# Kernel tuning notes

Measured on AMD Instinct MI355X. Metric: run time of the kernel, lower is better.

The kernel has to match this reference:

```python
import jax, jax.numpy as jnp
import numpy as np

D_MODEL = 1024
H = 16
D_K = D_MODEL // H


def setup_inputs() -> dict:
    key = jax.random.key(0)
    ks = jax.random.split(key, 12)
    B, S = 2, 2048
    inp = {
        "q": jax.random.normal(ks[0], (B, S, D_MODEL), jnp.float32),
        "k": jax.random.normal(ks[1], (B, S, D_MODEL), jnp.float32),
        "v": jax.random.normal(ks[2], (B, S, D_MODEL), jnp.float32),
        "mask": jax.random.randint(ks[3], (1, 1, S, S), 0, 2, jnp.int32),
    }
    s = 1.0 / np.sqrt(D_MODEL)
    inp["wq_w"] = jax.random.normal(ks[4], (D_MODEL, D_MODEL), jnp.float32) * s
    inp["wq_b"] = jnp.zeros((D_MODEL,), jnp.float32)
    inp["wk_w"] = jax.random.normal(ks[5], (D_MODEL, D_MODEL), jnp.float32) * s
    inp["wk_b"] = jnp.zeros((D_MODEL,), jnp.float32)
    inp["wv_w"] = jax.random.normal(ks[6], (D_MODEL, D_MODEL), jnp.float32) * s
    inp["wv_b"] = jnp.zeros((D_MODEL,), jnp.float32)
    inp["wo_w"] = jax.random.normal(ks[7], (D_MODEL, D_MODEL), jnp.float32) * s
    inp["wo_b"] = jnp.zeros((D_MODEL,), jnp.float32)
    return inp


def reference(q, k, v, mask, wq_w, wq_b, wk_w, wk_b, wv_w, wv_b, wo_w, wo_b):
    B, S, _ = q.shape
    # projections (torch Linear: x @ W^T + b)
    def proj(x, w, b):
        y = x @ w.T + b
        return y.reshape(B, S, H, D_K).transpose(0, 2, 1, 3)  # [B,H,S,Dk]

    Q = proj(q, wq_w, wq_b)
    K = proj(k, wk_w, wk_b)
    V = proj(v, wv_w, wv_b)

    scores = jnp.einsum("bhqd,bhkd->bhqk", Q, K) / jnp.sqrt(jnp.float32(D_K))
    # source quirk: masked positions set to 1e-9 (NOT -inf) before softmax
    scores = jnp.where(mask == 0, jnp.float32(1e-9), scores)
    attn = jax.nn.softmax(scores, axis=-1)
    out = jnp.einsum("bhqk,bhkd->bhqd", attn, V)
    out = out.transpose(0, 2, 1, 3).reshape(B, S, H * D_K)
    return out @ wo_w.T + wo_b
```

## Files before the change

### kernel.cpp

```cpp
#include <hip/hip_runtime.h>

typedef _Float16 half_t;
typedef _Float16 h8 __attribute__((ext_vector_type(8)));
typedef _Float16 h4 __attribute__((ext_vector_type(4)));
typedef _Float16 h2 __attribute__((ext_vector_type(2)));
typedef float f32x4 __attribute__((ext_vector_type(4)));
typedef float f32x16 __attribute__((ext_vector_type(16)));

#define S_LEN 2048
#define DMODEL 1024
#define NHEAD 16
#define HDK 64
#define NB 2
#define MROWS (NB * S_LEN)
#define LOG2E 1.44269504089f

__device__ __forceinline__ void gload_lds16(const void* g, void* l) {
  __builtin_amdgcn_global_load_lds(
      (const __attribute__((address_space(1))) unsigned int*)g,
      (__attribute__((address_space(3))) unsigned int*)l, 16, 0, 0);
}

__device__ __forceinline__ float fast_exp2(float x) {
  float r;
  asm("v_exp_f32 %0, %1" : "=v"(r) : "v"(x));
  return r;
}

__device__ __forceinline__ int swz(int row, int colByte) {
  return row * 128 + (colByte ^ ((row & 7) << 4));
}

__global__ __launch_bounds__(256) void pre_kernel(
    const float* __restrict__ q, const float* __restrict__ k, const float* __restrict__ v,
    const float* __restrict__ wq, const float* __restrict__ wk,
    const float* __restrict__ wv, const float* __restrict__ wo,
    const int* __restrict__ mask,
    half_t* Xq, half_t* Xk, half_t* Xv,
    half_t* Wq, half_t* Wk, half_t* Wv, half_t* Wo,
    unsigned int* mbits) {
  const int gid = blockIdx.x, tid = threadIdx.x;
  if (gid < 16384) {
    int i = gid * 256 + tid;
    const float* src; half_t* dst; int off;
    if (i < 3145728) {
      int rgn = i >> 20; off = i & 1048575;
      src = rgn == 0 ? q : rgn == 1 ? k : v;
      dst = rgn == 0 ? Xq : rgn == 1 ? Xk : Xv;
    } else {
      int j = i - 3145728;
      int rgn = j >> 18; off = j & 262143;
      src = rgn == 0 ? wq : rgn == 1 ? wk : rgn == 2 ? wv : wo;
      dst = rgn == 0 ? Wq : rgn == 1 ? Wk : rgn == 2 ? Wv : Wo;
    }
    float4 vv = ((const float4*)src)[off];
    h4 o;
    o[0] = (half_t)vv.x; o[1] = (half_t)vv.y; o[2] = (half_t)vv.z; o[3] = (half_t)vv.w;
    ((h4*)dst)[off] = o;
  } else {
    int i = (gid - 16384) * 256 + tid;
    int mv = mask[i];
    unsigned long long bm = __ballot(mv != 0);
    int lane = tid & 63;
    if (lane == 0)       mbits[i >> 5] = (unsigned int)bm;
    else if (lane == 32) mbits[i >> 5] = (unsigned int)(bm >> 32);
  }
}

template <int EPI>
__global__ __launch_bounds__(256) void gemm_kernel(
    const half_t* __restrict__ A0, const half_t* __restrict__ A1, const half_t* __restrict__ A2,
    const half_t* __restrict__ W0, const half_t* __restrict__ W1, const half_t* __restrict__ W2,
    const float* __restrict__ b0, const float* __restrict__ b1, const float* __restrict__ b2,
    void* o0, void* o1, void* o2) {
  const int nwg = gridDim.x;
  const int cpx = nwg >> 3;
  const int id = blockIdx.x;
  const int nid = (id & 7) * cpx + (id >> 3);
  const int z = nid >> 8;
  const int rmn = nid & 255;
  const int bm = rmn >> 3, bn = rmn & 7;

  const half_t* A; const half_t* W; const float* bias; void* out; float scale;
  if (z == 0)      { A = A0; W = W0; bias = b0; out = o0; scale = (EPI == 0) ? 0.125f * LOG2E : 1.0f; }
  else if (z == 1) { A = A1; W = W1; bias = b1; out = o1; scale = 1.0f; }
  else             { A = A2; W = W2; bias = b2; out = o2; scale = 1.0f; }

  __shared__ half_t As[2][128 * 32];
  __shared__ half_t Bs[2][128 * 32];
  const int tid = threadIdx.x;
  const int w = tid >> 6, lane = tid & 63;
  const int wm = w >> 1, wn = w & 1;
  const int crow = lane >> 2;
  const int ckb = ((lane & 3) * 16) ^ ((crow & 3) << 4);

  f32x4 acc[4][4] = {};

  const char* Ar0 = (const char*)A + (size_t)(bm * 128 + w * 16 + crow) * 2048 + ckb;
  const char* Ar1 = Ar0 + 64 * 2048;
  const char* Wr0 = (const char*)W + (size_t)(bn * 128 + w * 16 + crow) * 2048 + ckb;
  const char* Wr1 = Wr0 + 64 * 2048;

  const int rr = lane & 15;
  const int kkB = (lane >> 4) * 16;
  const int kswz = (rr & 3) << 4;

#define GSTAGE(buf, ktB)                                     \
  do {                                                       \
    gload_lds16(Ar0 + (ktB), As[buf] + w * 512);             \
    gload_lds16(Ar1 + (ktB), As[buf] + (w + 4) * 512);       \
    gload_lds16(Wr0 + (ktB), Bs[buf] + w * 512);             \
    gload_lds16(Wr1 + (ktB), Bs[buf] + (w + 4) * 512);       \
  } while (0)

  GSTAGE(0, 0);
  __syncthreads();

  int cur = 0;
  for (int ktB = 0; ktB < 2048; ktB += 64) {
    if (ktB + 64 < 2048) GSTAGE(cur ^ 1, ktB + 64);

    const char* AsB = (const char*)As[cur];
    const char* BsB = (const char*)Bs[cur];
    h8 af[4], bf[4];
#pragma unroll
    for (int i = 0; i < 4; ++i) {
      af[i] = *(const h8*)(AsB + (wm * 64 + i * 16 + rr) * 64 + (kkB ^ kswz));
      bf[i] = *(const h8*)(BsB + (wn * 64 + i * 16 + rr) * 64 + (kkB ^ kswz));
    }
#pragma unroll
    for (int i = 0; i < 4; ++i)
#pragma unroll
      for (int j = 0; j < 4; ++j)
        acc[i][j] = __builtin_amdgcn_mfma_f32_16x16x32_f16(af[i], bf[j], acc[i][j], 0, 0, 0);

    __syncthreads();
    cur ^= 1;
  }
#undef GSTAGE

  const int r0 = bm * 128 + wm * 64;
  const int c0 = bn * 128 + wn * 64;
#pragma unroll
  for (int j = 0; j < 4; ++j) {
    int col = c0 + j * 16 + (lane & 15);
    float bc = bias[col];
#pragma unroll
    for (int i = 0; i < 4; ++i) {
#pragma unroll
      for (int jj = 0; jj < 4; ++jj) {
        int row = r0 + i * 16 + (lane >> 4) * 4 + jj;
        float val = acc[i][j][jj] + bc;
        if (EPI == 0) {
          int bb = row >> 11, s = row & (S_LEN - 1);
          int hh = col >> 6, dk = col & 63;
          if (z == 2) {
            ((half_t*)out)[((size_t)((bb * NHEAD + hh) * HDK + dk)) * S_LEN + s] = (half_t)val;
          } else {
            ((half_t*)out)[(((size_t)(bb * NHEAD + hh)) * S_LEN + s) * HDK + dk] =
                (half_t)(val * scale);
          }
        } else {
          ((float*)out)[(size_t)row * DMODEL + col] = val;
        }
      }
    }
  }
}

__global__ __launch_bounds__(256, 4) void attn_kernel(
    const half_t* __restrict__ Qp, const half_t* __restrict__ Kp,
    const half_t* __restrict__ VTp, const unsigned int* __restrict__ mbits,
    half_t* __restrict__ AO) {
  __shared__ char smem[32768];

  const int tid = threadIdx.x, w = tid >> 6, lane = tid & 63;
  const int qg = w >> 1, kh = w & 1;
  const int id = blockIdx.x;
  const int xcd = id & 7, rest = id >> 3;
  const int bh = (xcd << 2) | (rest >> 5);
  const int qt = rest & 31;
  const int b = bh >> 4, h = bh & 15;
  const int q32 = lane & 31, hi = lane >> 5;
  const int qbase = qt * 64 + qg * 32;
  const half_t* Qb = Qp + (size_t)bh * (S_LEN * HDK);
  const char* Kb = (const char*)(Kp + (size_t)bh * (S_LEN * HDK));
  const char* VTb = (const char*)(VTp + (size_t)bh * (S_LEN * HDK));
  const unsigned int* mrow = mbits + (size_t)(qbase + q32) * (S_LEN / 32);

  char* Ks = smem;
  char* Vs = smem + 16384;
  const int srow = w * 16 + (lane >> 3);
  const int scb = (lane & 7) * 16;

  h8 qf[4];
#pragma unroll
  for (int s = 0; s < 4; ++s)
    qf[s] = *(const h8*)(Qb + (size_t)(qbase + q32) * HDK + s * 16 + hi * 8);

  f32x16 acc0 = {}, acc1 = {};
  float l_run = 0.f;

  unsigned int mw = mrow[kh];
#pragma unroll
  for (int p = 0; p < 2; ++p) {
    int r = srow + p * 8;
    gload_lds16(Kb + (size_t)r * 128 + (scb ^ ((r & 7) << 4)),
                Ks + (w * 16 + p * 8) * 128);
    gload_lds16(VTb + (size_t)r * (S_LEN * 2) + (scb ^ ((r & 7) << 4)),
                Vs + (w * 16 + p * 8) * 128);
  }
  __syncthreads();

  int cur = 0;
  for (int t = 0; t < 32; ++t) {
    const unsigned int mwc = mw >> (hi * 4);

    if (t < 31) {
      const int kvn = t + 1;
#pragma unroll
      for (int p = 0; p < 2; ++p) {
        int r = srow + p * 8;
        gload_lds16(Kb + (size_t)(kvn * 64 + r) * 128 + (scb ^ ((r & 7) << 4)),
                    Ks + (cur ^ 1) * 8192 + (w * 16 + p * 8) * 128);
        gload_lds16(VTb + (size_t)r * (S_LEN * 2) + kvn * 128 + (scb ^ ((r & 7) << 4)),
                    Vs + (cur ^ 1) * 8192 + (w * 16 + p * 8) * 128);
      }
      mw = mrow[kvn * 2 + kh];
    }

    const char* kb = Ks + cur * 8192;
    const char* vb = Vs + cur * 8192;
    f32x16 sc = {};
    __builtin_amdgcn_s_setprio(1);
#pragma unroll
    for (int s = 0; s < 4; ++s) {
      h8 kf = *(const h8*)(kb + swz(kh * 32 + q32, s * 32 + hi * 16));
      sc = __builtin_amdgcn_mfma_f32_32x32x16_f16(kf, qf[s], sc, 0, 0, 0);
    }
    __builtin_amdgcn_s_setprio(0);

    h8 vf00 = *(const h8*)(vb + swz(q32, kh * 64 + hi * 16));
    h8 vf01 = *(const h8*)(vb + swz(q32, kh * 64 + 32 + hi * 16));
    h8 vf10 = *(const h8*)(vb + swz(32 + q32, kh * 64 + hi * 16));
    h8 vf11 = *(const h8*)(vb + swz(32 + q32, kh * 64 + 32 + hi * 16));

#pragma unroll
    for (int rg = 0; rg < 16; ++rg) {
      const int bit = (rg & 3) + 8 * (rg >> 2);
      float p = fast_exp2(((mwc >> bit) & 1u) ? sc[rg] : 0.0f);
      sc[rg] = p;
      l_run += p;
    }

    h8 pb[2];
#pragma unroll
    for (int s = 0; s < 2; ++s) {
      const int rb = s * 8;
      union { h2 h; unsigned int u; } c01, c23, c45, c67;
      c01.h[0] = (half_t)sc[rb + 0]; c01.h[1] = (half_t)sc[rb + 1];
      c23.h[0] = (half_t)sc[rb + 2]; c23.h[1] = (half_t)sc[rb + 3];
      c45.h[0] = (half_t)sc[rb + 4]; c45.h[1] = (half_t)sc[rb + 5];
      c67.h[0] = (half_t)sc[rb + 6]; c67.h[1] = (half_t)sc[rb + 7];
      auto rA = __builtin_amdgcn_permlane32_swap(c01.u, c45.u, false, false);
      auto rB = __builtin_amdgcn_permlane32_swap(c23.u, c67.u, false, false);
      union { unsigned int u[4]; h8 v; } bw;
      bw.u[0] = rA[0]; bw.u[1] = rB[0]; bw.u[2] = rA[1]; bw.u[3] = rB[1];
      pb[s] = bw.v;
    }

    __builtin_amdgcn_s_setprio(1);
    acc0 = __builtin_amdgcn_mfma_f32_32x32x16_f16(vf00, pb[0], acc0, 0, 0, 0);
    acc1 = __builtin_amdgcn_mfma_f32_32x32x16_f16(vf10, pb[0], acc1, 0, 0, 0);
    acc0 = __builtin_amdgcn_mfma_f32_32x32x16_f16(vf01, pb[1], acc0, 0, 0, 0);
    acc1 = __builtin_amdgcn_mfma_f32_32x32x16_f16(vf11, pb[1], acc1, 0, 0, 0);
    __builtin_amdgcn_s_setprio(0);

    __syncthreads();
    cur ^= 1;
  }

  float* my = (float*)smem + (qg * 64 + lane) * 33;
  if (kh) {
#pragma unroll
    for (int rg = 0; rg < 16; ++rg) { my[rg] = acc0[rg]; my[16 + rg] = acc1[rg]; }
    my[32] = l_run;
  }
  __syncthreads();
  if (!kh) {
#pragma unroll
    for (int rg = 0; rg < 16; ++rg) { acc0[rg] += my[rg]; acc1[rg] += my[16 + rg]; }
    l_run += my[32];
    l_run += __shfl_xor(l_run, 32);

    const float inv = 1.0f / l_run;
    const int qrow = qbase + q32;
    half_t* aob = AO + (size_t)(b * S_LEN + qrow) * DMODEL + h * HDK;
#pragma unroll
    for (int rq = 0; rq < 4; ++rq) {
      h4 s0, s1;
#pragma unroll
      for (int j = 0; j < 4; ++j) {
        s0[j] = (half_t)(acc0[rq * 4 + j] * inv);
        s1[j] = (half_t)(acc1[rq * 4 + j] * inv);
      }
      const int d0 = 8 * rq + 4 * hi;
      *(h4*)(aob + d0) = s0;
      *(h4*)(aob + 32 + d0) = s1;
    }
  }
}

extern "C" void kernel_launch(void* const* d_in, const int* in_sizes, int n_in,
                              void* d_out, int out_size, void* d_ws, size_t ws_size,
                              hipStream_t stream) {
  const float* q    = (const float*)d_in[0];
  const float* k    = (const float*)d_in[1];
  const float* v    = (const float*)d_in[2];
  const int*   mask = (const int*)d_in[3];
  const float* wq_w = (const float*)d_in[4];
  const float* wq_b = (const float*)d_in[5];
  const float* wk_w = (const float*)d_in[6];
  const float* wk_b = (const float*)d_in[7];
  const float* wv_w = (const float*)d_in[8];
  const float* wv_b = (const float*)d_in[9];
  const float* wo_w = (const float*)d_in[10];
  const float* wo_b = (const float*)d_in[11];
  float* out = (float*)d_out;

  char* ws = (char*)d_ws;
  const size_t MB = (size_t)1 << 20;
  half_t* Xq = (half_t*)(ws + 0 * MB);
  half_t* Xk = (half_t*)(ws + 8 * MB);
  half_t* Xv = (half_t*)(ws + 16 * MB);
  half_t* Wq = (half_t*)(ws + 24 * MB);
  half_t* Wk = (half_t*)(ws + 26 * MB);
  half_t* Wv = (half_t*)(ws + 28 * MB);
  half_t* Wo = (half_t*)(ws + 30 * MB);
  half_t* Qp = (half_t*)(ws + 32 * MB);
  half_t* Kp = (half_t*)(ws + 40 * MB);
  half_t* VT = (half_t*)(ws + 48 * MB);
  unsigned int* mbits = (unsigned int*)(ws + 56 * MB);
  half_t* AO = Xq;

  pre_kernel<<<32768, 256, 0, stream>>>(q, k, v, wq_w, wk_w, wv_w, wo_w, mask,
                                        Xq, Xk, Xv, Wq, Wk, Wv, Wo, mbits);
  gemm_kernel<0><<<768, 256, 0, stream>>>(
      Xq, Xk, Xv, Wq, Wk, Wv, wq_b, wk_b, wv_b, (void*)Qp, (void*)Kp, (void*)VT);
  attn_kernel<<<1024, 256, 0, stream>>>(Qp, Kp, VT, mbits, AO);
  gemm_kernel<1><<<256, 256, 0, stream>>>(
      AO, AO, AO, Wo, Wo, Wo, wo_b, wo_b, wo_b, (void*)out, (void*)out, (void*)out);

  (void)in_sizes; (void)n_in; (void)out_size; (void)ws_size;
}
```

Measured before the change: 152.2 us.

## Coalesce V-transpose epilogue via LDS, transpose mask bits, split output GEMM tile

The V projection epilogue now stages the tile in swizzled LDS and writes the transposed V in 16-byte coalesced chunks, instead of scattered 2-byte stores. The mask bitmap is stored transposed so that adjacent query rows read adjacent words in the attention kernel. The output projection gets its own 64x128 tile kernel with 512 blocks for better CU occupancy. The P conversion uses packed cvt_pkrtz, which rounds toward zero and can change numerics slightly.

```diff
diff --git a/kernel.cpp b/kernel.cpp
--- a/kernel.cpp
+++ b/kernel.cpp
@@ -4,6 +4,7 @@
 typedef _Float16 h8 __attribute__((ext_vector_type(8)));
 typedef _Float16 h4 __attribute__((ext_vector_type(4)));
 typedef _Float16 h2 __attribute__((ext_vector_type(2)));
+typedef __fp16 fp16x2 __attribute__((ext_vector_type(2)));
 typedef float f32x4 __attribute__((ext_vector_type(4)));
 typedef float f32x16 __attribute__((ext_vector_type(16)));
 
@@ -12,7 +13,6 @@
 #define NHEAD 16
 #define HDK 64
 #define NB 2
-#define MROWS (NB * S_LEN)
 #define LOG2E 1.44269504089f
 
 __device__ __forceinline__ void gload_lds16(const void* g, void* l) {
@@ -38,7 +38,7 @@
     const int* __restrict__ mask,
     half_t* Xq, half_t* Xk, half_t* Xv,
     half_t* Wq, half_t* Wk, half_t* Wv, half_t* Wo,
-    unsigned int* mbits) {
+    unsigned int* mbT) {
   const int gid = blockIdx.x, tid = threadIdx.x;
   if (gid < 16384) {
     int i = gid * 256 + tid;
@@ -62,12 +62,13 @@
     int mv = mask[i];
     unsigned long long bm = __ballot(mv != 0);
     int lane = tid & 63;
-    if (lane == 0)       mbits[i >> 5] = (unsigned int)bm;
-    else if (lane == 32) mbits[i >> 5] = (unsigned int)(bm >> 32);
-  }
-}
-
-template <int EPI>
+    int widx = ((i >> 5) & 63);
+    int qrow = i >> 11;
+    if (lane == 0)       mbT[widx * S_LEN + qrow] = (unsigned int)bm;
+    else if (lane == 32) mbT[widx * S_LEN + qrow] = (unsigned int)(bm >> 32);
+  }
+}
+
 __global__ __launch_bounds__(256) void gemm_kernel(
     const half_t* __restrict__ A0, const half_t* __restrict__ A1, const half_t* __restrict__ A2,
     const half_t* __restrict__ W0, const half_t* __restrict__ W1, const half_t* __restrict__ W2,
@@ -82,12 +83,14 @@
   const int bm = rmn >> 3, bn = rmn & 7;
 
   const half_t* A; const half_t* W; const float* bias; void* out; float scale;
-  if (z == 0)      { A = A0; W = W0; bias = b0; out = o0; scale = (EPI == 0) ? 0.125f * LOG2E : 1.0f; }
+  if (z == 0)      { A = A0; W = W0; bias = b0; out = o0; scale = 0.125f * LOG2E; }
   else if (z == 1) { A = A1; W = W1; bias = b1; out = o1; scale = 1.0f; }
   else             { A = A2; W = W2; bias = b2; out = o2; scale = 1.0f; }
 
-  __shared__ half_t As[2][128 * 32];
-  __shared__ half_t Bs[2][128 * 32];
+  __shared__ char gsm[32768];
+#define ASB(buf) (gsm + (buf) * 8192)
+#define BSB(buf) (gsm + 16384 + (buf) * 8192)
+
   const int tid = threadIdx.x;
   const int w = tid >> 6, lane = tid & 63;
   const int wm = w >> 1, wn = w & 1;
@@ -107,10 +110,10 @@
 
 #define GSTAGE(buf, ktB)                                     \
   do {                                                       \
-    gload_lds16(Ar0 + (ktB), As[buf] + w * 512);             \
-    gload_lds16(Ar1 + (ktB), As[buf] + (w + 4) * 512);       \
-    gload_lds16(Wr0 + (ktB), Bs[buf] + w * 512);             \
-    gload_lds16(Wr1 + (ktB), Bs[buf] + (w + 4) * 512);       \
+    gload_lds16(Ar0 + (ktB), ASB(buf) + w * 1024);           \
+    gload_lds16(Ar1 + (ktB), ASB(buf) + (w + 4) * 1024);     \
+    gload_lds16(Wr0 + (ktB), BSB(buf) + w * 1024);           \
+    gload_lds16(Wr1 + (ktB), BSB(buf) + (w + 4) * 1024);     \
   } while (0)
 
   GSTAGE(0, 0);
@@ -120,8 +123,8 @@
   for (int ktB = 0; ktB < 2048; ktB += 64) {
     if (ktB + 64 < 2048) GSTAGE(cur ^ 1, ktB + 64);
 
-    const char* AsB = (const char*)As[cur];
-    const char* BsB = (const char*)Bs[cur];
+    const char* AsB = ASB(cur);
+    const char* BsB = BSB(cur);
     h8 af[4], bf[4];
 #pragma unroll
     for (int i = 0; i < 4; ++i) {
@@ -139,30 +142,139 @@
   }
 #undef GSTAGE
 
-  const int r0 = bm * 128 + wm * 64;
+  const int c0 = bn * 128;
+  if (z == 2) {
+    char* Ct = gsm;
+    const int g4 = (lane >> 4) * 4;
+#pragma unroll
+    for (int j = 0; j < 4; ++j) {
+      const int lcol = wn * 64 + j * 16 + rr;
+      const float bc = bias[c0 + lcol];
+      const int cswz = (lcol & 15) << 4;
+      char* colp = Ct + lcol * 256;
+#pragma unroll
+      for (int i = 0; i < 4; ++i) {
+#pragma unroll
+        for (int jj = 0; jj < 4; jj += 2) {
+          const int lrow = wm * 64 + i * 16 + g4 + jj;
+          union { h2 hh; unsigned u; } t;
+          t.hh[0] = (half_t)(acc[i][j][jj] + bc);
+          t.hh[1] = (half_t)(acc[i][j][jj + 1] + bc);
+          *(unsigned*)(colp + ((2 * lrow) ^ cswz)) = t.u;
+        }
+      }
+    }
+    __syncthreads();
+    const int col = tid >> 1, hf = tid & 1;
+    const int bb = bm >> 4, s0 = (bm & 15) * 128;
+    const int hh2 = (c0 + col) >> 6, dk = (c0 + col) & 63;
+    half_t* dst = (half_t*)out +
+        ((size_t)((bb * NHEAD + hh2) * HDK + dk)) * S_LEN + s0 + hf * 64;
+    const int cswz = (col & 15) << 4;
+    const char* colp = Ct + col * 256;
+#pragma unroll
+    for (int c = 0; c < 8; ++c) {
+      const int chunk = hf * 8 + c;
+      h8 vv = *(const h8*)(colp + ((chunk * 16) ^ cswz));
+      *(h8*)(dst + c * 8) = vv;
+    }
+  } else {
+    const int r0 = bm * 128 + wm * 64;
+#pragma unroll
+    for (int j = 0; j < 4; ++j) {
+      int col = c0 + wn * 64 + j * 16 + rr;
+      float bc = bias[col];
+#pragma unroll
+      for (int i = 0; i < 4; ++i) {
+#pragma unroll
+        for (int jj = 0; jj < 4; ++jj) {
+          int row = r0 + i * 16 + (lane >> 4) * 4 + jj;
+          float val = (acc[i][j][jj] + bc) * scale;
+          int bb = row >> 11, s = row & (S_LEN - 1);
+          int hh = col >> 6, dk = col & 63;
+          ((half_t*)out)[(((size_t)(bb * NHEAD + hh)) * S_LEN + s) * HDK + dk] = (half_t)val;
+        }
+      }
+    }
+  }
+#undef ASB
+#undef BSB
+}
+
+__global__ __launch_bounds__(256) void gemm_o_kernel(
+    const half_t* __restrict__ A, const half_t* __restrict__ W,
+    const float* __restrict__ bias, float* __restrict__ out) {
+  const int id = blockIdx.x;
+  const int nid = (id & 7) * 64 + (id >> 3);
+  const int bm = nid >> 3, bn = nid & 7;
+
+  __shared__ char gsm[24576];
+#define OSB(buf) (gsm + (buf) * 4096)
+#define OBB(buf) (gsm + 8192 + (buf) * 8192)
+
+  const int tid = threadIdx.x, w = tid >> 6, lane = tid & 63;
+  const int wm = w >> 1, wn = w & 1;
+  const int crow = lane >> 2;
+  const int ckb = ((lane & 3) * 16) ^ ((crow & 3) << 4);
+
+  f32x4 acc[2][4] = {};
+
+  const char* Ar = (const char*)A + (size_t)(bm * 64 + w * 16 + crow) * 2048 + ckb;
+  const char* Wr0 = (const char*)W + (size_t)(bn * 128 + w * 16 + crow) * 2048 + ckb;
+  const char* Wr1 = Wr0 + 64 * 2048;
+
+  const int rr = lane & 15;
+  const int kkB = (lane >> 4) * 16;
+  const int kswz = (rr & 3) << 4;
+
+#define OST(buf, ktB)                                      \
+  do {                                                     \
+    gload_lds16(Ar + (ktB), OSB(buf) + w * 1024);          \
+    gload_lds16(Wr0 + (ktB), OBB(buf) + w * 1024);         \
+    gload_lds16(Wr1 + (ktB), OBB(buf) + (w + 4) * 1024);   \
+  } while (0)
+
+  OST(0, 0);
+  __syncthreads();
+
+  int cur = 0;
+  for (int ktB = 0; ktB < 2048; ktB += 64) {
+    if (ktB + 64 < 2048) OST(cur ^ 1, ktB + 64);
+
+    const char* AsB = OSB(cur);
+    const char* BsB = OBB(cur);
+    h8 af[2], bf[4];
+#pragma unroll
+    for (int i = 0; i < 2; ++i)
+      af[i] = *(const h8*)(AsB + (wm * 32 + i * 16 + rr) * 64 + (kkB ^ kswz));
+#pragma unroll
+    for (int j = 0; j < 4; ++j)
+      bf[j] = *(const h8*)(BsB + (wn * 64 + j * 16 + rr) * 64 + (kkB ^ kswz));
+#pragma unroll
+    for (int i = 0; i < 2; ++i)
+#pragma unroll
+      for (int j = 0; j < 4; ++j)
+        acc[i][j] = __builtin_amdgcn_mfma_f32_16x16x32_f16(af[i], bf[j], acc[i][j], 0, 0, 0);
+
+    __syncthreads();
+    cur ^= 1;
+  }
+#undef OST
+#undef OSB
+#undef OBB
+
+  const int r0 = bm * 64 + wm * 32;
   const int c0 = bn * 128 + wn * 64;
 #pragma unroll
   for (int j = 0; j < 4; ++j) {
-    int col = c0 + j * 16 + (lane & 15);
+    int col = c0 + j * 16 + rr;
     float bc = bias[col];
 #pragma unroll
-    for (int i = 0; i < 4; ++i) {
+    for (int i = 0; i < 2; ++i) {
 #pragma unroll
       for (int jj = 0; jj < 4; ++jj) {
         int row = r0 + i * 16 + (lane >> 4) * 4 + jj;
-        float val = acc[i][j][jj] + bc;
-        if (EPI == 0) {
-          int bb = row >> 11, s = row & (S_LEN - 1);
-          int hh = col >> 6, dk = col & 63;
-          if (z == 2) {
-            ((half_t*)out)[((size_t)((bb * NHEAD + hh) * HDK + dk)) * S_LEN + s] = (half_t)val;
-          } else {
-            ((half_t*)out)[(((size_t)(bb * NHEAD + hh)) * S_LEN + s) * HDK + dk] =
-                (half_t)(val * scale);
-          }
-        } else {
-          ((float*)out)[(size_t)row * DMODEL + col] = val;
-        }
+        out[(size_t)row * DMODEL + col] = acc[i][j][jj] + bc;
       }
     }
   }
@@ -170,7 +282,7 @@
 
 __global__ __launch_bounds__(256, 4) void attn_kernel(
     const half_t* __restrict__ Qp, const half_t* __restrict__ Kp,
-    const half_t* __restrict__ VTp, const unsigned int* __restrict__ mbits,
+    const half_t* __restrict__ VTp, const unsigned int* __restrict__ mbT,
     half_t* __restrict__ AO) {
   __shared__ char smem[32768];
 
@@ -183,10 +295,10 @@
   const int b = bh >> 4, h = bh & 15;
   const int q32 = lane & 31, hi = lane >> 5;
   const int qbase = qt * 64 + qg * 32;
+  const int qrowIdx = qbase + q32;
   const half_t* Qb = Qp + (size_t)bh * (S_LEN * HDK);
   const char* Kb = (const char*)(Kp + (size_t)bh * (S_LEN * HDK));
   const char* VTb = (const char*)(VTp + (size_t)bh * (S_LEN * HDK));
-  const unsigned int* mrow = mbits + (size_t)(qbase + q32) * (S_LEN / 32);
 
   char* Ks = smem;
   char* Vs = smem + 16384;
@@ -196,12 +308,12 @@
   h8 qf[4];
 #pragma unroll
   for (int s = 0; s < 4; ++s)
-    qf[s] = *(const h8*)(Qb + (size_t)(qbase + q32) * HDK + s * 16 + hi * 8);
+    qf[s] = *(const h8*)(Qb + (size_t)qrowIdx * HDK + s * 16 + hi * 8);
 
   f32x16 acc0 = {}, acc1 = {};
   float l_run = 0.f;
 
-  unsigned int mw = mrow[kh];
+  unsigned int mw = mbT[(size_t)kh * S_LEN + qrowIdx];
 #pragma unroll
   for (int p = 0; p < 2; ++p) {
     int r = srow + p * 8;
@@ -226,7 +338,7 @@
         gload_lds16(VTb + (size_t)r * (S_LEN * 2) + kvn * 128 + (scb ^ ((r & 7) << 4)),
                     Vs + (cur ^ 1) * 8192 + (w * 16 + p * 8) * 128);
       }
-      mw = mrow[kvn * 2 + kh];
+      mw = mbT[(size_t)(kvn * 2 + kh) * S_LEN + qrowIdx];
     }
 
     const char* kb = Ks + cur * 8192;
@@ -257,16 +369,16 @@
 #pragma unroll
     for (int s = 0; s < 2; ++s) {
       const int rb = s * 8;
-      union { h2 h; unsigned int u; } c01, c23, c45, c67;
-      c01.h[0] = (half_t)sc[rb + 0]; c01.h[1] = (half_t)sc[rb + 1];
-      c23.h[0] = (half_t)sc[rb + 2]; c23.h[1] = (half_t)sc[rb + 3];
-      c45.h[0] = (half_t)sc[rb + 4]; c45.h[1] = (half_t)sc[rb + 5];
-      c67.h[0] = (half_t)sc[rb + 6]; c67.h[1] = (half_t)sc[rb + 7];
+      union { fp16x2 hh; unsigned u; } c01, c23, c45, c67;
+      c01.hh = __builtin_amdgcn_cvt_pkrtz(sc[rb + 0], sc[rb + 1]);
+      c23.hh = __builtin_amdgcn_cvt_pkrtz(sc[rb + 2], sc[rb + 3]);
+      c45.hh = __builtin_amdgcn_cvt_pkrtz(sc[rb + 4], sc[rb + 5]);
+      c67.hh = __builtin_amdgcn_cvt_pkrtz(sc[rb + 6], sc[rb + 7]);
       auto rA = __builtin_amdgcn_permlane32_swap(c01.u, c45.u, false, false);
       auto rB = __builtin_amdgcn_permlane32_swap(c23.u, c67.u, false, false);
-      union { unsigned int u[4]; h8 v; } bw;
+      union { unsigned int u[4]; h8 v_; } bw;
       bw.u[0] = rA[0]; bw.u[1] = rB[0]; bw.u[2] = rA[1]; bw.u[3] = rB[1];
-      pb[s] = bw.v;
+      pb[s] = bw.v_;
     }
 
     __builtin_amdgcn_s_setprio(1);
@@ -294,8 +406,7 @@
     l_run += __shfl_xor(l_run, 32);
 
     const float inv = 1.0f / l_run;
-    const int qrow = qbase + q32;
-    half_t* aob = AO + (size_t)(b * S_LEN + qrow) * DMODEL + h * HDK;
+    half_t* aob = AO + (size_t)(b * S_LEN + qrowIdx) * DMODEL + h * HDK;
 #pragma unroll
     for (int rq = 0; rq < 4; ++rq) {
       h4 s0, s1;
@@ -340,16 +451,15 @@
   half_t* Qp = (half_t*)(ws + 32 * MB);
   half_t* Kp = (half_t*)(ws + 40 * MB);
   half_t* VT = (half_t*)(ws + 48 * MB);
-  unsigned int* mbits = (unsigned int*)(ws + 56 * MB);
+  unsigned int* mbT = (unsigned int*)(ws + 56 * MB);
   half_t* AO = Xq;
 
   pre_kernel<<<32768, 256, 0, stream>>>(q, k, v, wq_w, wk_w, wv_w, wo_w, mask,
-                                        Xq, Xk, Xv, Wq, Wk, Wv, Wo, mbits);
-  gemm_kernel<0><<<768, 256, 0, stream>>>(
+                                        Xq, Xk, Xv, Wq, Wk, Wv, Wo, mbT);
+  gemm_kernel<<<768, 256, 0, stream>>>(
       Xq, Xk, Xv, Wq, Wk, Wv, wq_b, wk_b, wv_b, (void*)Qp, (void*)Kp, (void*)VT);
-  attn_kernel<<<1024, 256, 0, stream>>>(Qp, Kp, VT, mbits, AO);
-  gemm_kernel<1><<<256, 256, 0, stream>>>(
-      AO, AO, AO, Wo, Wo, Wo, wo_b, wo_b, wo_b, (void*)out, (void*)out, (void*)out);
+  attn_kernel<<<1024, 256, 0, stream>>>(Qp, Kp, VT, mbT, AO);
+  gemm_o_kernel<<<512, 256, 0, stream>>>(AO, Wo, wo_b, out);
 
   (void)in_sizes; (void)n_in; (void)out_size; (void)ws_size;
 }
```

Measured after the change: 142.4 us. -6.5%, faster.
